# Optimization experiments

Measured on AMD Instinct MI355X. Metric: run time of the kernel, lower is better.

The kernel has to match this reference:

```python
import jax, jax.numpy as jnp
import numpy as np
from jax import lax

N = 25600      # total nodes = G * T
E = 204800     # edges (before self loops)
IN_CH = 6
HID = 64
HEADS = 4
G = 512        # graphs per batch
T = 50         # sequence length (node_time in [0, T))
OUT = 30       # prediction_horizon * 3
NEG_SLOPE = 0.2
BN_EPS = 1e-5


def _gat(x, src, dst, W, a_src, a_dst, b, heads, outc):
    # PyG GATConv (concat=True): h = x W reshaped to (N, H, C)
    n = x.shape[0]
    h = (x @ W).reshape(n, heads, outc)
    # edge scores: leaky_relu(a_src . h_src + a_dst . h_dst), softmax over incoming edges of dst
    e = jax.nn.leaky_relu((h * a_src).sum(-1)[src] + (h * a_dst).sum(-1)[dst], NEG_SLOPE)  # (E, H)
    m = jax.ops.segment_max(e, dst, num_segments=n)
    ex = jnp.exp(e - m[dst])
    denom = jax.ops.segment_sum(ex, dst, num_segments=n)
    alpha = ex / denom[dst]
    out = jax.ops.segment_sum(alpha[:, :, None] * h[src], dst, num_segments=n)  # (N, H, C)
    return out.reshape(n, heads * outc) + b


def _bn_eval(x, g, b):
    # BatchNorm in eval with running_mean=0, running_var=1
    return g * (x * (1.0 / np.float32(np.sqrt(1.0 + BN_EPS)))) + b


def setup_inputs() -> dict:
    ks = jax.random.split(jax.random.key(0), 16)
    s = 0.1
    d = {}
    d["x"] = jax.random.normal(ks[0], (N, IN_CH), jnp.float32)
    d["edge_index"] = jax.random.randint(ks[1], (2, E), 0, N)
    idx = jnp.arange(N)
    d["batch"] = idx // T       # each graph has exactly T nodes
    d["node_time"] = idx % T
    d["W1"] = jax.random.normal(ks[2], (IN_CH, HEADS * HID), jnp.float32) * s
    d["att_src1"] = jax.random.normal(ks[3], (HEADS, HID), jnp.float32) * s
    d["att_dst1"] = jax.random.normal(ks[4], (HEADS, HID), jnp.float32) * s
    d["b1"] = jnp.zeros((HEADS * HID,), jnp.float32)
    d["g1"] = jnp.ones((HEADS * HID,), jnp.float32)
    d["be1"] = jnp.zeros((HEADS * HID,), jnp.float32)
    d["W2"] = jax.random.normal(ks[5], (HEADS * HID, HID), jnp.float32) * s
    d["att_src2"] = jax.random.normal(ks[6], (1, HID), jnp.float32) * s
    d["att_dst2"] = jax.random.normal(ks[7], (1, HID), jnp.float32) * s
    d["b2"] = jnp.zeros((HID,), jnp.float32)
    d["g2"] = jnp.ones((HID,), jnp.float32)
    d["be2"] = jnp.zeros((HID,), jnp.float32)
    d["Wih"] = jax.random.normal(ks[8], (4 * HID, HID), jnp.float32) * s
    d["Whh"] = jax.random.normal(ks[9], (4 * HID, HID), jnp.float32) * s
    d["bih"] = jnp.zeros((4 * HID,), jnp.float32)
    d["bhh"] = jnp.zeros((4 * HID,), jnp.float32)
    d["Wfc"] = jax.random.normal(ks[10], (HID, OUT), jnp.float32) * s
    d["bfc"] = jnp.zeros((OUT,), jnp.float32)
    return d


def reference(x, edge_index, batch, node_time, W1, att_src1, att_dst1, b1, g1, be1,
              W2, att_src2, att_dst2, b2, g2, be2, Wih, Whh, bih, bhh, Wfc, bfc):
    loops = jnp.arange(N)
    src = jnp.concatenate([edge_index[0], loops])  # GATConv adds self loops
    dst = jnp.concatenate([edge_index[1], loops])
    h = jax.nn.elu(_bn_eval(_gat(x, src, dst, W1, att_src1, att_dst1, b1, HEADS, HID), g1, be1))
    h = jax.nn.elu(_bn_eval(_gat(h, src, dst, W2, att_src2, att_dst2, b2, 1, HID), g2, be2))
    # vectorized replacement of the per-node python scatter loop
    x_seq = jnp.zeros((G, T, HID), h.dtype).at[batch, node_time].set(h)

    def step(carry, xt):
        hh, cc = carry
        gates = xt @ Wih.T + bih + hh @ Whh.T + bhh
        i, f, gg, o = jnp.split(gates, 4, axis=-1)
        cc = jax.nn.sigmoid(f) * cc + jax.nn.sigmoid(i) * jnp.tanh(gg)
        hh = jax.nn.sigmoid(o) * jnp.tanh(cc)
        return (hh, cc), None

    init = (jnp.zeros((G, HID), h.dtype), jnp.zeros((G, HID), h.dtype))
    (hn, _), _ = lax.scan(step, init, x_seq.transpose(1, 0, 2))  # scan over time
    return hn @ Wfc + bfc  # (G, 30)
```

## Files before the change

### kernel.cpp

```cpp
#include <hip/hip_runtime.h>

#define N_NODES 25600
#define N_EDGES 204800
#define EE (N_EDGES + N_NODES)
#define IN_CH 6
#define HID 64
#define HEADS 4
#define G_GRAPHS 512
#define T_STEPS 50
#define OUT_DIM 30
#define NEG_SLOPE 0.2f
#define BN_INV 0.9999950000374997f

__device__ __forceinline__ float lrelu_(float x){ return x > 0.f ? x : NEG_SLOPE * x; }
__device__ __forceinline__ float elu_(float x){ return x > 0.f ? x : __expf(x) - 1.f; }
__device__ __forceinline__ float sigmoid_(float x){
    return __builtin_amdgcn_rcpf(1.f + __expf(-x));
}
__device__ __forceinline__ float tanh_(float x){
    return 1.f - 2.f * __builtin_amdgcn_rcpf(1.f + __expf(2.f * x));
}
__device__ __forceinline__ float bcast_(float v, int l){
    return __int_as_float(__builtin_amdgcn_readlane(__float_as_int(v), l));
}

__global__ void count_k(const int* __restrict__ ei, int* __restrict__ counts){
    int e = blockIdx.x * 256 + threadIdx.x;
    if (e >= EE) return;
    int dst = (e < N_EDGES) ? ei[N_EDGES + e] : (e - N_EDGES);
    atomicAdd(&counts[dst], 1);
}

__global__ void scan_k(const int* __restrict__ counts, int* __restrict__ row_ptr,
                       int* __restrict__ cursor){
    __shared__ int part[1024];
    int t = threadIdx.x;
    const int CH = N_NODES / 1024;
    int base = t * CH;
    int s = 0;
    for (int i = 0; i < CH; i++) s += counts[base + i];
    part[t] = s;
    __syncthreads();
    for (int off = 1; off < 1024; off <<= 1){
        int v = (t >= off) ? part[t - off] : 0;
        __syncthreads();
        part[t] += v;
        __syncthreads();
    }
    int run = (t > 0) ? part[t - 1] : 0;
    for (int i = 0; i < CH; i++){
        int cv = counts[base + i];
        row_ptr[base + i] = run;
        cursor[base + i]  = run;
        run += cv;
    }
    if (t == 1023) row_ptr[N_NODES] = run;
}

__global__ void scatter_k(const int* __restrict__ ei, int* __restrict__ cursor,
                          int* __restrict__ ssrc){
    int e = blockIdx.x * 256 + threadIdx.x;
    if (e >= EE) return;
    int src, dst;
    if (e < N_EDGES){ src = ei[e]; dst = ei[N_EDGES + e]; }
    else            { src = dst = e - N_EDGES; }
    int pos = atomicAdd(&cursor[dst], 1);
    ssrc[pos] = src;
}

__global__ void gat1_tr(const float* __restrict__ x, const float* __restrict__ W1,
                        const float* __restrict__ asw, const float* __restrict__ adw,
                        float* __restrict__ h1_pre, float* __restrict__ as1,
                        float* __restrict__ ad1){
    __shared__ float w[IN_CH * 256];
    int tid = threadIdx.x;
    for (int i = tid; i < IN_CH * 256; i += 256) w[i] = W1[i];
    __syncthreads();
    int wv = tid >> 6, lane = tid & 63;
    int n = blockIdx.x * 4 + wv;
    float xv[IN_CH];
    #pragma unroll
    for (int k = 0; k < IN_CH; k++) xv[k] = x[n * IN_CH + k];
    float sA[4], sD[4];
    #pragma unroll
    for (int h = 0; h < 4; h++){
        int col = h * 64 + lane;
        float acc = 0.f;
        #pragma unroll
        for (int k = 0; k < IN_CH; k++) acc += xv[k] * w[k * 256 + col];
        h1_pre[n * 256 + col] = acc;
        sA[h] = acc * asw[col];
        sD[h] = acc * adw[col];
    }
    #pragma unroll
    for (int h = 0; h < 4; h++){
        #pragma unroll
        for (int off = 32; off; off >>= 1){
            sA[h] += __shfl_xor(sA[h], off);
            sD[h] += __shfl_xor(sD[h], off);
        }
    }
    if (lane == 0){
        *(float4*)&as1[n * 4] = make_float4(sA[0], sA[1], sA[2], sA[3]);
        *(float4*)&ad1[n * 4] = make_float4(sD[0], sD[1], sD[2], sD[3]);
    }
}

__global__ void gat1_agg(const float* __restrict__ h1_pre, const float* __restrict__ as1,
                         const float* __restrict__ ad1, const int* __restrict__ row_ptr,
                         const int* __restrict__ ssrc,
                         const float* __restrict__ b1, const float* __restrict__ g1,
                         const float* __restrict__ be1, float* __restrict__ h1_act){
    int wv = threadIdx.x >> 6, lane = threadIdx.x & 63;
    int n = blockIdx.x * 4 + wv;
    int s0 = row_ptr[n], s1 = row_ptr[n + 1];
    float4 adn = *(const float4*)&ad1[n * 4];
    float d0 = 0.f, d1 = 0.f, d2 = 0.f, d3 = 0.f;
    float a0 = 0.f, a1 = 0.f, a2 = 0.f, a3 = 0.f;
    for (int j = s0; j < s1; j++){
        int s = ssrc[j];
        float4 as = *(const float4*)&as1[s * 4];
        float e0 = __expf(lrelu_(as.x + adn.x));
        float e1 = __expf(lrelu_(as.y + adn.y));
        float e2 = __expf(lrelu_(as.z + adn.z));
        float e3 = __expf(lrelu_(as.w + adn.w));
        d0 += e0; d1 += e1; d2 += e2; d3 += e3;
        const float* hp = h1_pre + (size_t)s * 256;
        a0 += e0 * hp[lane];
        a1 += e1 * hp[64 + lane];
        a2 += e2 * hp[128 + lane];
        a3 += e3 * hp[192 + lane];
    }
    float accs[4] = {a0 / d0, a1 / d1, a2 / d2, a3 / d3};
    #pragma unroll
    for (int h = 0; h < 4; h++){
        int col = h * 64 + lane;
        float v = accs[h] + b1[col];
        v = g1[col] * (v * BN_INV) + be1[col];
        h1_act[(size_t)n * 256 + col] = elu_(v);
    }
}

#define TM 64
#define KT 32
#define APAD 4
__global__ __launch_bounds__(256) void gat2_tr(const float* __restrict__ h1_act,
                        const float* __restrict__ W2,
                        const float* __restrict__ asw, const float* __restrict__ adw,
                        float* __restrict__ h2_pre, float* __restrict__ as2,
                        float* __restrict__ ad2){
    __shared__ float As[TM][KT + APAD];
    __shared__ float Bs[KT][64];
    int tx = threadIdx.x;
    int rg = tx >> 4;
    int cg = tx & 15;
    int r0 = rg * 4, c0 = cg * 4;
    int rowBase = blockIdx.x * TM;
    float acc[4][4] = {};
    for (int k0 = 0; k0 < 256; k0 += KT){
        #pragma unroll
        for (int it = 0; it < 2; it++){
            int i = tx + it * 256;
            int row = i >> 3;
            int c4  = (i & 7) * 4;
            *(float4*)&As[row][c4] =
                *(const float4*)(h1_act + (size_t)(rowBase + row) * 256 + k0 + c4);
        }
        #pragma unroll
        for (int it = 0; it < 2; it++){
            int i = tx + it * 256;
            int row = i >> 4;
            int c4  = (i & 15) * 4;
            *(float4*)&Bs[row][c4] = *(const float4*)(W2 + (size_t)(k0 + row) * 64 + c4);
        }
        __syncthreads();
        #pragma unroll
        for (int kq = 0; kq < KT; kq += 4){
            float4 b0 = *(float4*)&Bs[kq + 0][c0];
            float4 b1v = *(float4*)&Bs[kq + 1][c0];
            float4 b2v = *(float4*)&Bs[kq + 2][c0];
            float4 b3 = *(float4*)&Bs[kq + 3][c0];
            #pragma unroll
            for (int i = 0; i < 4; i++){
                float4 a = *(float4*)&As[r0 + i][kq];
                acc[i][0] += a.x * b0.x + a.y * b1v.x + a.z * b2v.x + a.w * b3.x;
                acc[i][1] += a.x * b0.y + a.y * b1v.y + a.z * b2v.y + a.w * b3.y;
                acc[i][2] += a.x * b0.z + a.y * b1v.z + a.z * b2v.z + a.w * b3.z;
                acc[i][3] += a.x * b0.w + a.y * b1v.w + a.z * b2v.w + a.w * b3.w;
            }
        }
        __syncthreads();
    }
    float aw0 = asw[c0], aw1 = asw[c0+1], aw2 = asw[c0+2], aw3 = asw[c0+3];
    float dw0 = adw[c0], dw1 = adw[c0+1], dw2 = adw[c0+2], dw3 = adw[c0+3];
    #pragma unroll
    for (int i = 0; i < 4; i++){
        int row = rowBase + r0 + i;
        *(float4*)(h2_pre + (size_t)row * 64 + c0) =
            make_float4(acc[i][0], acc[i][1], acc[i][2], acc[i][3]);
        float sA = acc[i][0]*aw0 + acc[i][1]*aw1 + acc[i][2]*aw2 + acc[i][3]*aw3;
        float sD = acc[i][0]*dw0 + acc[i][1]*dw1 + acc[i][2]*dw2 + acc[i][3]*dw3;
        #pragma unroll
        for (int off = 8; off; off >>= 1){
            sA += __shfl_xor(sA, off);
            sD += __shfl_xor(sD, off);
        }
        if (cg == 0){ as2[row] = sA; ad2[row] = sD; }
    }
}

__global__ void gat2_agg(const float* __restrict__ h2_pre, const float* __restrict__ as2,
                         const float* __restrict__ ad2, const int* __restrict__ row_ptr,
                         const int* __restrict__ ssrc,
                         const float* __restrict__ b2, const float* __restrict__ g2,
                         const float* __restrict__ be2,
                         const int* __restrict__ batch, const int* __restrict__ ntime,
                         float* __restrict__ xseq){
    int wv = threadIdx.x >> 6, lane = threadIdx.x & 63;
    int n = blockIdx.x * 4 + wv;
    int s0 = row_ptr[n], s1 = row_ptr[n + 1];
    float adn = ad2[n];
    float denom = 0.f, acc = 0.f;
    for (int j = s0; j < s1; j++){
        int s = ssrc[j];
        float e = __expf(lrelu_(as2[s] + adn));
        denom += e;
        acc += e * h2_pre[(size_t)s * 64 + lane];
    }
    float v = acc / denom + b2[lane];
    v = g2[lane] * (v * BN_INV) + be2[lane];
    v = elu_(v);
    int pos = batch[n] * T_STEPS + ntime[n];
    xseq[(size_t)pos * 64 + lane] = v;
}

__global__ __launch_bounds__(256) void gx_k(const float* __restrict__ xseq,
        const float* __restrict__ Wih, const float* __restrict__ bih,
        const float* __restrict__ bhh, float* __restrict__ gx){
    __shared__ float As[64][68];
    __shared__ float Bs[64][128];
    int tx = threadIdx.x;
    int rowBase = blockIdx.x * 64;
    int colBase = blockIdx.y * 128;
    #pragma unroll
    for (int it = 0; it < 4; it++){
        int i = tx + it * 256;
        int r = i >> 4;
        int c4 = (i & 15) * 4;
        *(float4*)&As[r][c4] = *(const float4*)(xseq + (size_t)(rowBase + r) * 64 + c4);
    }
    #pragma unroll
    for (int it = 0; it < 8; it++){
        int i = tx + it * 256;
        int jj = i & 127;
        int k4 = (i >> 7) * 4;
        float4 wv = *(const float4*)(Wih + (size_t)(colBase + jj) * 64 + k4);
        Bs[k4 + 0][jj] = wv.x;
        Bs[k4 + 1][jj] = wv.y;
        Bs[k4 + 2][jj] = wv.z;
        Bs[k4 + 3][jj] = wv.w;
    }
    __syncthreads();
    int rg = tx >> 5;
    int cg = tx & 31;
    int r0 = rg * 8, c0 = cg * 4;
    float acc[8][4] = {};
    #pragma unroll
    for (int kq = 0; kq < 64; kq += 4){
        float4 b0 = *(float4*)&Bs[kq + 0][c0];
        float4 b1 = *(float4*)&Bs[kq + 1][c0];
        float4 b2 = *(float4*)&Bs[kq + 2][c0];
        float4 b3 = *(float4*)&Bs[kq + 3][c0];
        #pragma unroll
        for (int i = 0; i < 8; i++){
            float4 a = *(float4*)&As[r0 + i][kq];
            acc[i][0] += a.x * b0.x + a.y * b1.x + a.z * b2.x + a.w * b3.x;
            acc[i][1] += a.x * b0.y + a.y * b1.y + a.z * b2.y + a.w * b3.y;
            acc[i][2] += a.x * b0.z + a.y * b1.z + a.z * b2.z + a.w * b3.z;
            acc[i][3] += a.x * b0.w + a.y * b1.w + a.z * b2.w + a.w * b3.w;
        }
    }
    int col = colBase + c0;
    float4 bb = make_float4(bih[col] + bhh[col], bih[col+1] + bhh[col+1],
                            bih[col+2] + bhh[col+2], bih[col+3] + bhh[col+3]);
    #pragma unroll
    for (int i = 0; i < 8; i++){
        int row = rowBase + r0 + i;
        *(float4*)(gx + (size_t)row * 256 + col) =
            make_float4(acc[i][0] + bb.x, acc[i][1] + bb.y,
                        acc[i][2] + bb.z, acc[i][3] + bb.w);
    }
}

__global__ __launch_bounds__(256, 2) void lstm_k(const float* __restrict__ gx,
        const float* __restrict__ Whh,
        const float* __restrict__ Wfc, const float* __restrict__ bfc,
        float* __restrict__ out){
    int g = blockIdx.x;
    int j = threadIdx.x;
    int lane = j & 63;
    __shared__ float gates[2][256];
    float4 whh[16];
    const float4* Hr = (const float4*)(Whh + j * 64);
    #pragma unroll
    for (int k = 0; k < 16; k++) whh[k] = Hr[k];
    float h = 0.f, c = 0.f;
    const float* gxg = gx + (size_t)g * T_STEPS * 256;
    float gxv = gxg[j];
    for (int t = 0; t < T_STEPS; t++){
        float gx_next = (t + 1 < T_STEPS) ? gxg[(t + 1) * 256 + j] : 0.f;
        float a0 = gxv, a1 = 0.f, a2 = 0.f, a3 = 0.f;
        #pragma unroll
        for (int k = 0; k < 16; k++){
            float4 wv = whh[k];
            a0 += wv.x * bcast_(h, 4 * k + 0);
            a1 += wv.y * bcast_(h, 4 * k + 1);
            a2 += wv.z * bcast_(h, 4 * k + 2);
            a3 += wv.w * bcast_(h, 4 * k + 3);
        }
        int buf = t & 1;
        gates[buf][j] = (a0 + a1) + (a2 + a3);
        __syncthreads();
        float iv = gates[buf][lane];
        float fv = gates[buf][64 + lane];
        float gv = gates[buf][128 + lane];
        float ov = gates[buf][192 + lane];
        c = sigmoid_(fv) * c + sigmoid_(iv) * tanh_(gv);
        h = sigmoid_(ov) * tanh_(c);
        gxv = gx_next;
    }
    if (j < 64) gates[0][j] = h;
    __syncthreads();
    if (j < OUT_DIM){
        float acc = bfc[j];
        #pragma unroll
        for (int k = 0; k < 64; k++) acc += gates[0][k] * Wfc[k * OUT_DIM + j];
        out[g * OUT_DIM + j] = acc;
    }
}

extern "C" void kernel_launch(void* const* d_in, const int* in_sizes, int n_in,
                              void* d_out, int out_size, void* d_ws, size_t ws_size,
                              hipStream_t stream){
    const float* x    = (const float*)d_in[0];
    const int*   ei   = (const int*)  d_in[1];
    const int*   batch= (const int*)  d_in[2];
    const int*   ntime= (const int*)  d_in[3];
    const float* W1   = (const float*)d_in[4];
    const float* as1w = (const float*)d_in[5];
    const float* ad1w = (const float*)d_in[6];
    const float* b1   = (const float*)d_in[7];
    const float* g1   = (const float*)d_in[8];
    const float* be1  = (const float*)d_in[9];
    const float* W2   = (const float*)d_in[10];
    const float* as2w = (const float*)d_in[11];
    const float* ad2w = (const float*)d_in[12];
    const float* b2   = (const float*)d_in[13];
    const float* g2   = (const float*)d_in[14];
    const float* be2  = (const float*)d_in[15];
    const float* Wih  = (const float*)d_in[16];
    const float* Whh  = (const float*)d_in[17];
    const float* bih  = (const float*)d_in[18];
    const float* bhh  = (const float*)d_in[19];
    const float* Wfc  = (const float*)d_in[20];
    const float* bfc  = (const float*)d_in[21];
    float* out = (float*)d_out;

    char* w = (char*)d_ws;
    auto alloc = [&](size_t bytes)->char*{
        char* p = w;
        w += (bytes + 255) & ~size_t(255);
        return p;
    };
    float* h1_pre = (float*)alloc((size_t)N_NODES * 256 * 4);
    float* h1_act = (float*)alloc((size_t)N_NODES * 256 * 4);
    float* h2_pre = (float*)alloc((size_t)N_NODES * 64 * 4);
    float* xseq   = (float*)alloc((size_t)G_GRAPHS * T_STEPS * 64 * 4);
    float* as1    = (float*)alloc((size_t)N_NODES * 4 * 4);
    float* ad1    = (float*)alloc((size_t)N_NODES * 4 * 4);
    float* as2    = (float*)alloc((size_t)N_NODES * 4);
    float* ad2    = (float*)alloc((size_t)N_NODES * 4);
    int* counts   = (int*)alloc((size_t)N_NODES * 4);
    int* row_ptr  = (int*)alloc((size_t)(N_NODES + 1) * 4);
    int* cursor   = (int*)alloc((size_t)N_NODES * 4);
    int* ssrc     = (int*)alloc((size_t)EE * 4);
    float* gx     = h1_pre;

    hipMemsetAsync(counts, 0, (size_t)N_NODES * 4, stream);
    count_k  <<<(EE + 255) / 256, 256, 0, stream>>>(ei, counts);
    scan_k   <<<1, 1024, 0, stream>>>(counts, row_ptr, cursor);
    scatter_k<<<(EE + 255) / 256, 256, 0, stream>>>(ei, cursor, ssrc);
    gat1_tr  <<<N_NODES / 4, 256, 0, stream>>>(x, W1, as1w, ad1w, h1_pre, as1, ad1);
    gat1_agg <<<N_NODES / 4, 256, 0, stream>>>(h1_pre, as1, ad1, row_ptr, ssrc, b1, g1, be1, h1_act);
    gat2_tr  <<<N_NODES / TM, 256, 0, stream>>>(h1_act, W2, as2w, ad2w, h2_pre, as2, ad2);
    gat2_agg <<<N_NODES / 4, 256, 0, stream>>>(h2_pre, as2, ad2, row_ptr, ssrc, b2, g2, be2, batch, ntime, xseq);
    gx_k     <<<dim3(N_NODES / 64, 2), 256, 0, stream>>>(xseq, Wih, bih, bhh, gx);
    lstm_k   <<<G_GRAPHS, 256, 0, stream>>>(gx, Whh, Wfc, bfc, out);
}
```

Before: 318.3 us.

## Aggregate raw 6-channel inputs before GAT1 projection and use LDS for LSTM hidden broadcast

GAT layer 1 now folds the attention vectors into W1 so per-node scores come straight from x. Messages are then aggregated over the 6-dim inputs and projected by W1 only after aggregation, using linearity. This removes the 26 MB h1_pre write and the 256-wide gathers per edge, replacing them with 6-float gathers and a small per-node matmul. The LSTM also replaces 64 readlane broadcasts per step with LDS float4 reads from a per-wave double-buffered hidden state, which adds LDS traffic.

Result: faster. 306.1 us (-3.8%).

```diff
diff --git a/kernel.cpp b/kernel.cpp
--- a/kernel.cpp
+++ b/kernel.cpp
@@ -19,9 +19,6 @@
 }
 __device__ __forceinline__ float tanh_(float x){
     return 1.f - 2.f * __builtin_amdgcn_rcpf(1.f + __expf(2.f * x));
-}
-__device__ __forceinline__ float bcast_(float v, int l){
-    return __int_as_float(__builtin_amdgcn_readlane(__float_as_int(v), l));
 }
 
 __global__ void count_k(const int* __restrict__ ei, int* __restrict__ counts){
@@ -68,55 +65,54 @@
     ssrc[pos] = src;
 }
 
-__global__ void gat1_tr(const float* __restrict__ x, const float* __restrict__ W1,
-                        const float* __restrict__ asw, const float* __restrict__ adw,
-                        float* __restrict__ h1_pre, float* __restrict__ as1,
-                        float* __restrict__ ad1){
-    __shared__ float w[IN_CH * 256];
+__global__ void wa_k(const float* __restrict__ W1, const float* __restrict__ asw,
+                     const float* __restrict__ adw, float* __restrict__ waS,
+                     float* __restrict__ waD){
+    int t = threadIdx.x;
+    if (t >= 48) return;
+    int k = t >> 3, h = (t >> 1) & 3, which = t & 1;
+    const float* a = which ? adw : asw;
+    float s = 0.f;
+    #pragma unroll
+    for (int c = 0; c < 64; c++) s += W1[k * 256 + h * 64 + c] * a[h * 64 + c];
+    (which ? waD : waS)[k * 4 + h] = s;
+}
+
+__global__ void ns_k(const float* __restrict__ x, const float* __restrict__ waS,
+                     const float* __restrict__ waD, float* __restrict__ as1,
+                     float* __restrict__ ad1){
+    int n = blockIdx.x * 256 + threadIdx.x;
+    float xv[IN_CH];
+    #pragma unroll
+    for (int k = 0; k < IN_CH; k++) xv[k] = x[n * IN_CH + k];
+    float sv[4] = {0.f, 0.f, 0.f, 0.f}, dv[4] = {0.f, 0.f, 0.f, 0.f};
+    #pragma unroll
+    for (int k = 0; k < IN_CH; k++){
+        #pragma unroll
+        for (int h = 0; h < 4; h++){
+            sv[h] += xv[k] * waS[k * 4 + h];
+            dv[h] += xv[k] * waD[k * 4 + h];
+        }
+    }
+    *(float4*)&as1[n * 4] = make_float4(sv[0], sv[1], sv[2], sv[3]);
+    *(float4*)&ad1[n * 4] = make_float4(dv[0], dv[1], dv[2], dv[3]);
+}
+
+__global__ void gat1_aggx(const float* __restrict__ x, const float* __restrict__ as1,
+                          const float* __restrict__ ad1, const int* __restrict__ row_ptr,
+                          const int* __restrict__ ssrc, const float* __restrict__ W1,
+                          const float* __restrict__ b1, const float* __restrict__ g1,
+                          const float* __restrict__ be1, float* __restrict__ h1_act){
+    __shared__ float w1s[IN_CH * 256];
     int tid = threadIdx.x;
-    for (int i = tid; i < IN_CH * 256; i += 256) w[i] = W1[i];
+    for (int i = tid; i < IN_CH * 256; i += 256) w1s[i] = W1[i];
     __syncthreads();
     int wv = tid >> 6, lane = tid & 63;
     int n = blockIdx.x * 4 + wv;
-    float xv[IN_CH];
-    #pragma unroll
-    for (int k = 0; k < IN_CH; k++) xv[k] = x[n * IN_CH + k];
-    float sA[4], sD[4];
-    #pragma unroll
-    for (int h = 0; h < 4; h++){
-        int col = h * 64 + lane;
-        float acc = 0.f;
-        #pragma unroll
-        for (int k = 0; k < IN_CH; k++) acc += xv[k] * w[k * 256 + col];
-        h1_pre[n * 256 + col] = acc;
-        sA[h] = acc * asw[col];
-        sD[h] = acc * adw[col];
-    }
-    #pragma unroll
-    for (int h = 0; h < 4; h++){
-        #pragma unroll
-        for (int off = 32; off; off >>= 1){
-            sA[h] += __shfl_xor(sA[h], off);
-            sD[h] += __shfl_xor(sD[h], off);
-        }
-    }
-    if (lane == 0){
-        *(float4*)&as1[n * 4] = make_float4(sA[0], sA[1], sA[2], sA[3]);
-        *(float4*)&ad1[n * 4] = make_float4(sD[0], sD[1], sD[2], sD[3]);
-    }
-}
-
-__global__ void gat1_agg(const float* __restrict__ h1_pre, const float* __restrict__ as1,
-                         const float* __restrict__ ad1, const int* __restrict__ row_ptr,
-                         const int* __restrict__ ssrc,
-                         const float* __restrict__ b1, const float* __restrict__ g1,
-                         const float* __restrict__ be1, float* __restrict__ h1_act){
-    int wv = threadIdx.x >> 6, lane = threadIdx.x & 63;
-    int n = blockIdx.x * 4 + wv;
     int s0 = row_ptr[n], s1 = row_ptr[n + 1];
     float4 adn = *(const float4*)&ad1[n * 4];
+    float xs0[IN_CH] = {}, xs1[IN_CH] = {}, xs2[IN_CH] = {}, xs3[IN_CH] = {};
     float d0 = 0.f, d1 = 0.f, d2 = 0.f, d3 = 0.f;
-    float a0 = 0.f, a1 = 0.f, a2 = 0.f, a3 = 0.f;
     for (int j = s0; j < s1; j++){
         int s = ssrc[j];
         float4 as = *(const float4*)&as1[s * 4];
@@ -125,17 +121,27 @@
         float e2 = __expf(lrelu_(as.z + adn.z));
         float e3 = __expf(lrelu_(as.w + adn.w));
         d0 += e0; d1 += e1; d2 += e2; d3 += e3;
-        const float* hp = h1_pre + (size_t)s * 256;
-        a0 += e0 * hp[lane];
-        a1 += e1 * hp[64 + lane];
-        a2 += e2 * hp[128 + lane];
-        a3 += e3 * hp[192 + lane];
-    }
-    float accs[4] = {a0 / d0, a1 / d1, a2 / d2, a3 / d3};
+        const float2* xp = (const float2*)(x + (size_t)s * IN_CH);
+        float2 xa = xp[0], xb = xp[1], xc = xp[2];
+        float xv[IN_CH] = {xa.x, xa.y, xb.x, xb.y, xc.x, xc.y};
+        #pragma unroll
+        for (int k = 0; k < IN_CH; k++){
+            xs0[k] += e0 * xv[k];
+            xs1[k] += e1 * xv[k];
+            xs2[k] += e2 * xv[k];
+            xs3[k] += e3 * xv[k];
+        }
+    }
+    float r0 = 1.f / d0, r1 = 1.f / d1, r2 = 1.f / d2, r3 = 1.f / d3;
     #pragma unroll
     for (int h = 0; h < 4; h++){
+        const float* xsh = (h == 0) ? xs0 : (h == 1) ? xs1 : (h == 2) ? xs2 : xs3;
+        float rh = (h == 0) ? r0 : (h == 1) ? r1 : (h == 2) ? r2 : r3;
         int col = h * 64 + lane;
-        float v = accs[h] + b1[col];
+        float acc = 0.f;
+        #pragma unroll
+        for (int k = 0; k < IN_CH; k++) acc += xsh[k] * w1s[k * 256 + col];
+        float v = acc * rh + b1[col];
         v = g1[col] * (v * BN_INV) + be1[col];
         h1_act[(size_t)n * 256 + col] = elu_(v);
     }
@@ -298,27 +304,32 @@
         float* __restrict__ out){
     int g = blockIdx.x;
     int j = threadIdx.x;
-    int lane = j & 63;
+    int wv = j >> 6, lane = j & 63;
     __shared__ float gates[2][256];
+    __shared__ float hb[4][2][64];
     float4 whh[16];
     const float4* Hr = (const float4*)(Whh + j * 64);
     #pragma unroll
     for (int k = 0; k < 16; k++) whh[k] = Hr[k];
-    float h = 0.f, c = 0.f;
+    float c = 0.f;
+    hb[wv][0][lane] = 0.f;
     const float* gxg = gx + (size_t)g * T_STEPS * 256;
     float gxv = gxg[j];
+    float hn = 0.f;
     for (int t = 0; t < T_STEPS; t++){
         float gx_next = (t + 1 < T_STEPS) ? gxg[(t + 1) * 256 + j] : 0.f;
+        int buf = t & 1;
+        const float4* hp = (const float4*)hb[wv][buf];
         float a0 = gxv, a1 = 0.f, a2 = 0.f, a3 = 0.f;
         #pragma unroll
         for (int k = 0; k < 16; k++){
-            float4 wv = whh[k];
-            a0 += wv.x * bcast_(h, 4 * k + 0);
-            a1 += wv.y * bcast_(h, 4 * k + 1);
-            a2 += wv.z * bcast_(h, 4 * k + 2);
-            a3 += wv.w * bcast_(h, 4 * k + 3);
-        }
-        int buf = t & 1;
+            float4 hv = hp[k];
+            float4 wvv = whh[k];
+            a0 += wvv.x * hv.x;
+            a1 += wvv.y * hv.y;
+            a2 += wvv.z * hv.z;
+            a3 += wvv.w * hv.w;
+        }
         gates[buf][j] = (a0 + a1) + (a2 + a3);
         __syncthreads();
         float iv = gates[buf][lane];
@@ -326,10 +337,11 @@
         float gv = gates[buf][128 + lane];
         float ov = gates[buf][192 + lane];
         c = sigmoid_(fv) * c + sigmoid_(iv) * tanh_(gv);
-        h = sigmoid_(ov) * tanh_(c);
+        hn = sigmoid_(ov) * tanh_(c);
+        hb[wv][buf ^ 1][lane] = hn;
         gxv = gx_next;
     }
-    if (j < 64) gates[0][j] = h;
+    if (wv == 0) gates[0][lane] = hn;
     __syncthreads();
     if (j < OUT_DIM){
         float acc = bfc[j];
@@ -372,26 +384,28 @@
         w += (bytes + 255) & ~size_t(255);
         return p;
     };
-    float* h1_pre = (float*)alloc((size_t)N_NODES * 256 * 4);
     float* h1_act = (float*)alloc((size_t)N_NODES * 256 * 4);
+    float* gx     = (float*)alloc((size_t)N_NODES * 256 * 4);
     float* h2_pre = (float*)alloc((size_t)N_NODES * 64 * 4);
     float* xseq   = (float*)alloc((size_t)G_GRAPHS * T_STEPS * 64 * 4);
     float* as1    = (float*)alloc((size_t)N_NODES * 4 * 4);
     float* ad1    = (float*)alloc((size_t)N_NODES * 4 * 4);
     float* as2    = (float*)alloc((size_t)N_NODES * 4);
     float* ad2    = (float*)alloc((size_t)N_NODES * 4);
+    float* waS    = (float*)alloc(IN_CH * 4 * 4);
+    float* waD    = (float*)alloc(IN_CH * 4 * 4);
     int* counts   = (int*)alloc((size_t)N_NODES * 4);
     int* row_ptr  = (int*)alloc((size_t)(N_NODES + 1) * 4);
     int* cursor   = (int*)alloc((size_t)N_NODES * 4);
     int* ssrc     = (int*)alloc((size_t)EE * 4);
-    float* gx     = h1_pre;
 
     hipMemsetAsync(counts, 0, (size_t)N_NODES * 4, stream);
     count_k  <<<(EE + 255) / 256, 256, 0, stream>>>(ei, counts);
     scan_k   <<<1, 1024, 0, stream>>>(counts, row_ptr, cursor);
     scatter_k<<<(EE + 255) / 256, 256, 0, stream>>>(ei, cursor, ssrc);
-    gat1_tr  <<<N_NODES / 4, 256, 0, stream>>>(x, W1, as1w, ad1w, h1_pre, as1, ad1);
-    gat1_agg <<<N_NODES / 4, 256, 0, stream>>>(h1_pre, as1, ad1, row_ptr, ssrc, b1, g1, be1, h1_act);
+    wa_k     <<<1, 64, 0, stream>>>(W1, as1w, ad1w, waS, waD);
+    ns_k     <<<N_NODES / 256, 256, 0, stream>>>(x, waS, waD, as1, ad1);
+    gat1_aggx<<<N_NODES / 4, 256, 0, stream>>>(x, as1, ad1, row_ptr, ssrc, W1, b1, g1, be1, h1_act);
     gat2_tr  <<<N_NODES / TM, 256, 0, stream>>>(h1_act, W2, as2w, ad2w, h2_pre, as2, ad2);
     gat2_agg <<<N_NODES / 4, 256, 0, stream>>>(h2_pre, as2, ad2, row_ptr, ssrc, b2, g2, be2, batch, ntime, xseq);
     gx_k     <<<dim3(N_NODES / 64, 2), 256, 0, stream>>>(xseq, Wih, bih, bhh, gx);
```
